# Kernel tuning notes

Hardware: AMD Instinct MI355X
Metric: run time of the kernel (lower is better)

## Reference

```python
import jax, jax.numpy as jnp
import numpy as np

BATCH, SEQ, IN, HID = 64, 256, 512, 1024
TAU = 0.5
SW = SU = SA = 0.05


def setup_inputs() -> dict:
    key = jax.random.key(0)
    ks = jax.random.split(key, 9)
    x = jax.random.normal(ks[0], (BATCH, SEQ, IN), dtype=jnp.float32)
    # layer 0: input_size -> hidden_size
    W0 = jax.random.normal(ks[1], (HID, IN), dtype=jnp.float32) * SW
    U0 = jax.random.normal(ks[2], (HID, HID), dtype=jnp.float32) * SU
    b0 = jnp.zeros((HID,), dtype=jnp.float32)
    a0 = jnp.ones((HID,), dtype=jnp.float32) * SA
    # layer 1: hidden_size -> hidden_size
    W1 = jax.random.normal(ks[3], (HID, HID), dtype=jnp.float32) * SW
    U1 = jax.random.normal(ks[4], (HID, HID), dtype=jnp.float32) * SU
    b1 = jnp.zeros((HID,), dtype=jnp.float32)
    a1 = jnp.ones((HID,), dtype=jnp.float32) * SA
    return {"x": x, "W0": W0, "U0": U0, "b0": b0, "alpha0": a0,
            "W1": W1, "U1": U1, "b1": b1, "alpha1": a1}


def _run(x, params):
    B = x.shape[0]
    H = params[0][1].shape[0]
    inv_tau = 1.0 / TAU

    def cell(x_t, h, W, U, b, a):
        # Euler step of liquid neuron ODE: dh = (-h + tanh(W x + U h + b)) / tau
        pre = jnp.tanh(x_t @ W.T + h @ U.T + b)
        return h + a * ((pre - h) * inv_tau)

    def step(hs, x_t):
        new_hs = []
        inp = x_t
        for (W, U, b, a), h in zip(params, hs):
            h = cell(inp, h, W, U, b, a)
            new_hs.append(h)
            inp = h
        return tuple(new_hs), None

    hs0 = tuple(jnp.zeros((B, H), x.dtype) for _ in params)
    hs_final, _ = jax.lax.scan(step, hs0, jnp.swapaxes(x, 0, 1))  # scan over time
    return hs_final[-1]  # (batch, hidden)


def reference(x, W0, U0, b0, alpha0, W1, U1, b1, alpha1):
    params = [(W0, U0, b0, alpha0), (W1, U1, b1, alpha1)]
    return _run(x, params)
```

## Files before the change

### kernel.cpp

```cpp
#include <hip/hip_runtime.h>


typedef _Float16 f16;
typedef _Float16 f16x4 __attribute__((ext_vector_type(4)));
typedef _Float16 f16x8 __attribute__((ext_vector_type(8)));
typedef float    f32x4 __attribute__((ext_vector_type(4)));

#define B_  64
#define S_  256
#define IN_ 512
#define H_  1024
#define GR_ 16

static constexpr size_t OFF_H0R = 0;
static constexpr size_t OFF_H1R = 1048576;
static constexpr size_t OFF_FLG = 2097152;

#define AGENT __HIP_MEMORY_SCOPE_AGENT

__device__ __forceinline__ void pollf2(const int* fA, int tA,
                                       const int* fB, int tB, int lane) {
  const bool a = (lane < 16) && (tA > 0);
  const bool b = (lane >= 16) && (lane < 32) && (tB > 0);
  const int* p = a ? (fA + lane) : (fB + (lane & 15));
  const int tgt = a ? tA : tB;
  bool pend = a || b;
  if (pend && __hip_atomic_load((int*)p, __ATOMIC_RELAXED, AGENT) >= tgt)
    pend = false;
  while (__ballot(pend)) {
    __builtin_amdgcn_s_sleep(1);
    if (pend && __hip_atomic_load((int*)p, __ATOMIC_RELAXED, AGENT) >= tgt)
      pend = false;
  }
}

__device__ __forceinline__ float fast_tanh(float x) {
  float t = __expf(-2.0f * fabsf(x));
  float r = (1.0f - t) / (1.0f + t);
  return copysignf(r, x);
}

__device__ __forceinline__ void slab16(const f16* __restrict__ A, int kbase,
                                       int l15, int q,
                                       const f16x8 (&Bf)[4][8], f32x4 (&acc)[4]) {
  f16x8 cur[8];
  const f16* ar = A + (size_t)l15 * H_ + kbase + q * 8;
#pragma unroll
  for (int kf = 0; kf < 8; ++kf) cur[kf] = *(const f16x8*)(ar + kf * 32);
#pragma unroll
  for (int nt = 0; nt < 4; ++nt)
#pragma unroll
    for (int kf = 0; kf < 8; ++kf)
      acc[nt] = __builtin_amdgcn_mfma_f32_16x16x32_f16(cur[kf], Bf[nt][kf],
                                                       acc[nt], 0, 0, 0);
}

__global__ __launch_bounds__(256, 1) void k_persist(
    const float* __restrict__ x,  const float* __restrict__ W0,
    const float* __restrict__ U0, const float* __restrict__ b0,
    const float* __restrict__ W1, const float* __restrict__ U1,
    const float* __restrict__ alpha0, const float* __restrict__ alpha1,
    const float* __restrict__ b1,
    f16* h0r, f16* h1r, int* flg, float* out) {
  __shared__ __attribute__((aligned(16))) float red[4][16][68];
  const int tid = threadIdx.x;
  const int w = tid >> 6, lane = tid & 63;
  const int q = lane >> 4, l15 = lane & 15;

  int* ecnt = flg + 1024;
  int* xgrp = flg + 1032;

  const int xcc = (int)__builtin_amdgcn_s_getreg(6164) & 7;
  int* sh = (int*)&red[0][0][0];
  if (tid == 0) {
    int my = __hip_atomic_fetch_add(ecnt + xcc, 1, __ATOMIC_RELAXED, AGENT);
    if (blockIdx.x == 0) {
      unsigned taken = 0; int assigned = 0;
      while (assigned < 4) {
        for (int i = 0; i < 8 && assigned < 4; ++i)
          if (!((taken >> i) & 1) &&
              __hip_atomic_load(ecnt + i, __ATOMIC_RELAXED, AGENT) >= 32) {
            taken |= 1u << i;
            __hip_atomic_store(xgrp + i, assigned + 1, __ATOMIC_RELAXED, AGENT);
            ++assigned;
          }
        if (assigned < 4) __builtin_amdgcn_s_sleep(1);
      }
      for (int i = 0; i < 8; ++i)
        if (!((taken >> i) & 1))
          __hip_atomic_store(xgrp + i, -1, __ATOMIC_RELAXED, AGENT);
    }
    int grp = -1;
    if (my < 32) {
      int v;
      while ((v = __hip_atomic_load(xgrp + xcc, __ATOMIC_RELAXED, AGENT)) == 0)
        __builtin_amdgcn_s_sleep(1);
      if (v > 0) grp = v - 1;
    }
    sh[0] = (grp >= 0) ? my : -1;
    sh[1] = grp;
  }
  __syncthreads();
  const int myid = sh[0], g = sh[1];
  __syncthreads();
  if (myid < 0) return;
  const int role = myid >> 4, slice = myid & 15;
  const int c0 = slice * 64;
  const int kbase = w * 256;
  const int kxbase = w * 128;

  int* flag0w = flg + g * 256;
  int* flag1w = flg + g * 256 + 16;
  f16* h0g = h0r + (size_t)g * 8 * GR_ * H_;
  f16* h1g = h1r + (size_t)g * 8 * GR_ * H_;

  f16x8 BfA[4][8];
  f16x8 BfB[4][8];
  f16x8 BfX[4][4];
  {
    const float* WmA = (role == 0) ? U0 : W1;
#pragma unroll
    for (int nt = 0; nt < 4; ++nt)
#pragma unroll
      for (int kf = 0; kf < 8; ++kf) {
        const float* p = WmA + (size_t)(c0 + nt * 16 + l15) * H_ + kbase + kf * 32 + q * 8;
        f16x8 v;
#pragma unroll
        for (int j = 0; j < 8; ++j) v[j] = (f16)p[j];
        BfA[nt][kf] = v;
      }
    if (role == 1) {
#pragma unroll
      for (int nt = 0; nt < 4; ++nt)
#pragma unroll
        for (int kf = 0; kf < 8; ++kf) {
          const float* p = U1 + (size_t)(c0 + nt * 16 + l15) * H_ + kbase + kf * 32 + q * 8;
          f16x8 v;
#pragma unroll
          for (int j = 0; j < 8; ++j) v[j] = (f16)p[j];
          BfB[nt][kf] = v;
        }
    } else {
#pragma unroll
      for (int nt = 0; nt < 4; ++nt)
#pragma unroll
        for (int kf = 0; kf < 4; ++kf) {
          const float* p = W0 + (size_t)(c0 + nt * 16 + l15) * IN_ + kxbase + kf * 32 + q * 8;
          f16x8 v;
#pragma unroll
          for (int j = 0; j < 8; ++j) v[j] = (f16)p[j];
          BfX[nt][kf] = v;
        }
    }
  }

  const int row16 = tid >> 4, cgrp = tid & 15;
  const int iidx  = (cgrp >> 2) * 4 + (row16 & 3);
  const int bcol  = (row16 >> 2) * 16 + ((((cgrp & 3) * 4)) ^ ((row16 & 3) << 2));
  const int coff  = c0 + cgrp * 4;
  const int bglob = g * GR_ + row16;

  float cf[4], bs[4];
  {
    const float* ap = ((role == 0) ? alpha0 : alpha1) + coff;
    const float* bp = ((role == 0) ? b0 : b1) + coff;
#pragma unroll
    for (int j = 0; j < 4; ++j) { cf[j] = ap[j] * 2.0f; bs[j] = bp[j]; }
  }

  float hst[4] = {0.f, 0.f, 0.f, 0.f};

  if (role == 0) {
    const float* xrow = x + ((size_t)(g * GR_ + l15) * S_) * IN_ + kxbase + q * 8;
    for (int s = 0; s < 256; ++s) {
      const float* xb = xrow + (size_t)s * IN_;
      float4 xv[4][2];
#pragma unroll
      for (int kf = 0; kf < 4; ++kf) {
        xv[kf][0] = *(const float4*)(xb + kf * 32);
        xv[kf][1] = *(const float4*)(xb + kf * 32 + 4);
      }
      f32x4 acc[4] = {};
      if (s > 0) {
        pollf2(flag0w, s, flag1w, s - 7, lane);
        slab16(h0g + (size_t)((s - 1) & 7) * GR_ * H_, kbase, l15, q, BfA, acc);
      }
      f16x8 ax[4];
#pragma unroll
      for (int kf = 0; kf < 4; ++kf) {
        f16x8 a;
        const float* v0 = (const float*)&xv[kf][0];
        const float* v1 = (const float*)&xv[kf][1];
#pragma unroll
        for (int j = 0; j < 4; ++j) { a[j] = (f16)v0[j]; a[4 + j] = (f16)v1[j]; }
        ax[kf] = a;
      }
#pragma unroll
      for (int nt = 0; nt < 4; ++nt)
#pragma unroll
        for (int kf = 0; kf < 4; ++kf)
          acc[nt] = __builtin_amdgcn_mfma_f32_16x16x32_f16(ax[kf], BfX[nt][kf],
                                                           acc[nt], 0, 0, 0);
#pragma unroll
      for (int nt = 0; nt < 4; ++nt)
#pragma unroll
        for (int r = 0; r < 4; ++r)
          red[w][nt * 4 + r][lane ^ (r << 2)] = acc[nt][r];
      __syncthreads();
      f32x4 vs = {};
#pragma unroll
      for (int ks = 0; ks < 4; ++ks) {
        f32x4 v = *(const f32x4*)&red[ks][iidx][bcol];
        vs[0] += v[0]; vs[1] += v[1]; vs[2] += v[2]; vs[3] += v[3];
      }
      f16* hw = h0g + (size_t)(s & 7) * GR_ * H_ + (size_t)row16 * H_ + coff;
      f16x4 o;
#pragma unroll
      for (int j = 0; j < 4; ++j) {
        float th = fast_tanh(vs[j] + bs[j]);
        float h = hst[j];
        h = h + cf[j] * (th - h);
        hst[j] = h;
        o[j] = (f16)h;
      }
      *(f16x4*)hw = o;
      __syncthreads();
      if (tid == 0)
        __hip_atomic_store(flag0w + slice, s + 1, __ATOMIC_RELAXED, AGENT);
    }
  } else {
    for (int t = 0; t < 256; ++t) {
      pollf2(flag0w, t + 1, flag1w, t, lane);
      f32x4 acc[4] = {};
      f16x8 cA[8], cB[8];
      const f16* a0 = h0g + (size_t)(t & 7) * GR_ * H_ + (size_t)l15 * H_ + kbase + q * 8;
#pragma unroll
      for (int kf = 0; kf < 8; ++kf) cA[kf] = *(const f16x8*)(a0 + kf * 32);
      if (t > 0) {
        const f16* a1 = h1g + (size_t)((t - 1) & 7) * GR_ * H_ + (size_t)l15 * H_ + kbase + q * 8;
#pragma unroll
        for (int kf = 0; kf < 8; ++kf) cB[kf] = *(const f16x8*)(a1 + kf * 32);
      }
#pragma unroll
      for (int nt = 0; nt < 4; ++nt)
#pragma unroll
        for (int kf = 0; kf < 8; ++kf)
          acc[nt] = __builtin_amdgcn_mfma_f32_16x16x32_f16(cA[kf], BfA[nt][kf],
                                                           acc[nt], 0, 0, 0);
      if (t > 0) {
#pragma unroll
        for (int nt = 0; nt < 4; ++nt)
#pragma unroll
          for (int kf = 0; kf < 8; ++kf)
            acc[nt] = __builtin_amdgcn_mfma_f32_16x16x32_f16(cB[kf], BfB[nt][kf],
                                                             acc[nt], 0, 0, 0);
      }
#pragma unroll
      for (int nt = 0; nt < 4; ++nt)
#pragma unroll
        for (int r = 0; r < 4; ++r)
          red[w][nt * 4 + r][lane ^ (r << 2)] = acc[nt][r];
      __syncthreads();
      f32x4 vs = {};
#pragma unroll
      for (int ks = 0; ks < 4; ++ks) {
        f32x4 v = *(const f32x4*)&red[ks][iidx][bcol];
        vs[0] += v[0]; vs[1] += v[1]; vs[2] += v[2]; vs[3] += v[3];
      }
      f16* hw = h1g + (size_t)(t & 7) * GR_ * H_ + (size_t)row16 * H_ + coff;
      f16x4 o;
#pragma unroll
      for (int j = 0; j < 4; ++j) {
        float th = fast_tanh(vs[j] + bs[j]);
        float h = hst[j];
        h = h + cf[j] * (th - h);
        hst[j] = h;
        o[j] = (f16)h;
      }
      *(f16x4*)hw = o;
      if (t == 255) {
        float* op = out + (size_t)bglob * H_ + coff;
        float4 vv;
        vv.x = hst[0]; vv.y = hst[1]; vv.z = hst[2]; vv.w = hst[3];
        *(float4*)op = vv;
      }
      __syncthreads();
      if (tid == 0)
        __hip_atomic_store(flag1w + slice, t + 1, __ATOMIC_RELAXED, AGENT);
    }
  }
}


extern "C" void kernel_launch(void* const* d_in, const int* in_sizes, int n_in,
                              void* d_out, int out_size, void* d_ws, size_t ws_size,
                              hipStream_t stream) {
  const float* x  = (const float*)d_in[0];
  const float* W0 = (const float*)d_in[1];
  const float* U0 = (const float*)d_in[2];
  const float* b0 = (const float*)d_in[3];
  const float* a0 = (const float*)d_in[4];
  const float* W1 = (const float*)d_in[5];
  const float* U1 = (const float*)d_in[6];
  const float* b1 = (const float*)d_in[7];
  const float* a1 = (const float*)d_in[8];
  char* ws = (char*)d_ws;
  f16*   h0r = (f16*)(ws + OFF_H0R);
  f16*   h1r = (f16*)(ws + OFF_H1R);
  int*   flg = (int*)(ws + OFF_FLG);
  float* out = (float*)d_out;

  hipMemsetAsync(flg, 0, 32768, stream);

  k_persist<<<256, 256, 0, stream>>>(x, W0, U0, b0, W1, U1, a0, a1, b1,
                                     h0r, h1r, flg, out);
}
```

Baseline: 1.033 ms.

## Use per-wave flags and double-buffered LDS to drop trailing block barrier

Replaces the per-block completion flag, set after a second __syncthreads, with per-wave flags (64 per layer per group). Each wave publishes its own flag after waiting for its global stores, and consumers poll all 64 lanes. The LDS reduction buffer is double-buffered by step parity so the trailing barrier can be removed safely. The layer-1 block now polls the layer-0 flag and the layer-1 flag separately, so the W1·h0 slab can start before the recurrent input is ready. This costs more flag words and polling traffic, and it relies on relaxed atomics plus vmcnt for ordering.

Result: slower. 1.185 ms (+14.7%).

```diff
diff --git a/kernel.cpp b/kernel.cpp
--- a/kernel.cpp
+++ b/kernel.cpp
@@ -18,20 +18,21 @@
 
 #define AGENT __HIP_MEMORY_SCOPE_AGENT
 
-__device__ __forceinline__ void pollf2(const int* fA, int tA,
-                                       const int* fB, int tB, int lane) {
-  const bool a = (lane < 16) && (tA > 0);
-  const bool b = (lane >= 16) && (lane < 32) && (tB > 0);
-  const int* p = a ? (fA + lane) : (fB + (lane & 15));
-  const int tgt = a ? tA : tB;
-  bool pend = a || b;
-  if (pend && __hip_atomic_load((int*)p, __ATOMIC_RELAXED, AGENT) >= tgt)
-    pend = false;
+__device__ __forceinline__ void pollf(const int* f, int tgt, int lane) {
+  if (tgt <= 0) return;
+  const int* p = f + lane;
+  bool pend = true;
+  if (__hip_atomic_load((int*)p, __ATOMIC_RELAXED, AGENT) >= tgt) pend = false;
   while (__ballot(pend)) {
     __builtin_amdgcn_s_sleep(1);
     if (pend && __hip_atomic_load((int*)p, __ATOMIC_RELAXED, AGENT) >= tgt)
       pend = false;
   }
+}
+
+__device__ __forceinline__ void publishw(int* word, int val, int lane) {
+  asm volatile("s_waitcnt vmcnt(0)" ::: "memory");
+  if (lane == 0) __hip_atomic_store(word, val, __ATOMIC_RELAXED, AGENT);
 }
 
 __device__ __forceinline__ float fast_tanh(float x) {
@@ -62,7 +63,7 @@
     const float* __restrict__ alpha0, const float* __restrict__ alpha1,
     const float* __restrict__ b1,
     f16* h0r, f16* h1r, int* flg, float* out) {
-  __shared__ __attribute__((aligned(16))) float red[4][16][68];
+  __shared__ __attribute__((aligned(16))) float red[2][4][16][68];
   const int tid = threadIdx.x;
   const int w = tid >> 6, lane = tid & 63;
   const int q = lane >> 4, l15 = lane & 15;
@@ -71,7 +72,7 @@
   int* xgrp = flg + 1032;
 
   const int xcc = (int)__builtin_amdgcn_s_getreg(6164) & 7;
-  int* sh = (int*)&red[0][0][0];
+  int* sh = (int*)&red[0][0][0][0];
   if (tid == 0) {
     int my = __hip_atomic_fetch_add(ecnt + xcc, 1, __ATOMIC_RELAXED, AGENT);
     if (blockIdx.x == 0) {
@@ -108,9 +109,10 @@
   const int c0 = slice * 64;
   const int kbase = w * 256;
   const int kxbase = w * 128;
+  const int wword = slice * 4 + w;
 
   int* flag0w = flg + g * 256;
-  int* flag1w = flg + g * 256 + 16;
+  int* flag1w = flg + g * 256 + 64;
   f16* h0g = h0r + (size_t)g * 8 * GR_ * H_;
   f16* h1g = h1r + (size_t)g * 8 * GR_ * H_;
 
@@ -182,7 +184,8 @@
       }
       f32x4 acc[4] = {};
       if (s > 0) {
-        pollf2(flag0w, s, flag1w, s - 7, lane);
+        pollf(flag0w, s, lane);
+        pollf(flag1w, s - 7, lane);
         slab16(h0g + (size_t)((s - 1) & 7) * GR_ * H_, kbase, l15, q, BfA, acc);
       }
       f16x8 ax[4];
@@ -201,16 +204,17 @@
         for (int kf = 0; kf < 4; ++kf)
           acc[nt] = __builtin_amdgcn_mfma_f32_16x16x32_f16(ax[kf], BfX[nt][kf],
                                                            acc[nt], 0, 0, 0);
+      float (*rb)[16][68] = red[s & 1];
 #pragma unroll
       for (int nt = 0; nt < 4; ++nt)
 #pragma unroll
         for (int r = 0; r < 4; ++r)
-          red[w][nt * 4 + r][lane ^ (r << 2)] = acc[nt][r];
+          rb[w][nt * 4 + r][lane ^ (r << 2)] = acc[nt][r];
       __syncthreads();
       f32x4 vs = {};
 #pragma unroll
       for (int ks = 0; ks < 4; ++ks) {
-        f32x4 v = *(const f32x4*)&red[ks][iidx][bcol];
+        f32x4 v = *(const f32x4*)&rb[ks][iidx][bcol];
         vs[0] += v[0]; vs[1] += v[1]; vs[2] += v[2]; vs[3] += v[3];
       }
       f16* hw = h0g + (size_t)(s & 7) * GR_ * H_ + (size_t)row16 * H_ + coff;
@@ -224,47 +228,28 @@
         o[j] = (f16)h;
       }
       *(f16x4*)hw = o;
-      __syncthreads();
-      if (tid == 0)
-        __hip_atomic_store(flag0w + slice, s + 1, __ATOMIC_RELAXED, AGENT);
+      publishw(flag0w + wword, s + 1, lane);
     }
   } else {
     for (int t = 0; t < 256; ++t) {
-      pollf2(flag0w, t + 1, flag1w, t, lane);
       f32x4 acc[4] = {};
-      f16x8 cA[8], cB[8];
-      const f16* a0 = h0g + (size_t)(t & 7) * GR_ * H_ + (size_t)l15 * H_ + kbase + q * 8;
-#pragma unroll
-      for (int kf = 0; kf < 8; ++kf) cA[kf] = *(const f16x8*)(a0 + kf * 32);
+      pollf(flag0w, t + 1, lane);
+      slab16(h0g + (size_t)(t & 7) * GR_ * H_, kbase, l15, q, BfA, acc);
       if (t > 0) {
-        const f16* a1 = h1g + (size_t)((t - 1) & 7) * GR_ * H_ + (size_t)l15 * H_ + kbase + q * 8;
-#pragma unroll
-        for (int kf = 0; kf < 8; ++kf) cB[kf] = *(const f16x8*)(a1 + kf * 32);
-      }
-#pragma unroll
-      for (int nt = 0; nt < 4; ++nt)
-#pragma unroll
-        for (int kf = 0; kf < 8; ++kf)
-          acc[nt] = __builtin_amdgcn_mfma_f32_16x16x32_f16(cA[kf], BfA[nt][kf],
-                                                           acc[nt], 0, 0, 0);
-      if (t > 0) {
-#pragma unroll
-        for (int nt = 0; nt < 4; ++nt)
-#pragma unroll
-          for (int kf = 0; kf < 8; ++kf)
-            acc[nt] = __builtin_amdgcn_mfma_f32_16x16x32_f16(cB[kf], BfB[nt][kf],
-                                                             acc[nt], 0, 0, 0);
-      }
+        pollf(flag1w, t, lane);
+        slab16(h1g + (size_t)((t - 1) & 7) * GR_ * H_, kbase, l15, q, BfB, acc);
+      }
+      float (*rb)[16][68] = red[t & 1];
 #pragma unroll
       for (int nt = 0; nt < 4; ++nt)
 #pragma unroll
         for (int r = 0; r < 4; ++r)
-          red[w][nt * 4 + r][lane ^ (r << 2)] = acc[nt][r];
+          rb[w][nt * 4 + r][lane ^ (r << 2)] = acc[nt][r];
       __syncthreads();
       f32x4 vs = {};
 #pragma unroll
       for (int ks = 0; ks < 4; ++ks) {
-        f32x4 v = *(const f32x4*)&red[ks][iidx][bcol];
+        f32x4 v = *(const f32x4*)&rb[ks][iidx][bcol];
         vs[0] += v[0]; vs[1] += v[1]; vs[2] += v[2]; vs[3] += v[3];
       }
       f16* hw = h1g + (size_t)(t & 7) * GR_ * H_ + (size_t)row16 * H_ + coff;
@@ -284,9 +269,7 @@
         vv.x = hst[0]; vv.y = hst[1]; vv.z = hst[2]; vv.w = hst[3];
         *(float4*)op = vv;
       }
-      __syncthreads();
-      if (tid == 0)
-        __hip_atomic_store(flag1w + slice, t + 1, __ATOMIC_RELAXED, AGENT);
+      publishw(flag1w + wword, t + 1, lane);
     }
   }
 }
```
